# Performance work log

Measured on AMD Instinct MI355X. Metric: run time of the kernel, lower is better.

## Reference

```python
import jax, jax.numpy as jnp
import numpy as np

H = 8  # heads hardcoded in LightGFormer


def layernorm(x, g, b, eps=1e-5):
    m = x.mean(-1, keepdims=True)
    v = ((x - m) ** 2).mean(-1, keepdims=True)
    return (x - m) / jnp.sqrt(v + eps) * g + b


def setup_inputs() -> dict:
    key = jax.random.key(0)
    B, N, D, L = 16, 512, 256, 4
    Dff = 4 * D
    ks = jax.random.split(key, 12)

    def w(k, shape, scale=0.02):
        return jax.random.normal(k, shape, jnp.float32) * scale

    return {
        "input": w(ks[0], (B, N, D), 1.0),
        "input_v": w(ks[1], (B, N, D), 1.0),
        "pos_emb": w(ks[2], (N, D)),
        "Wq": w(ks[3], (L, D, D)), "bq": jnp.zeros((L, D), jnp.float32),
        "Wk": w(ks[4], (L, D, D)), "bk": jnp.zeros((L, D), jnp.float32),
        "Wv": w(ks[5], (L, D, D)), "bv": jnp.zeros((L, D), jnp.float32),
        "Wo": w(ks[6], (L, D, D)), "bo": jnp.zeros((L, D), jnp.float32),
        "W1": w(ks[7], (L, D, Dff)), "b1": jnp.zeros((L, Dff), jnp.float32),
        "W2": w(ks[8], (L, Dff // 2, D // 2)), "b2": jnp.zeros((L, D // 2), jnp.float32),
        "g1": jnp.ones((L, D), jnp.float32), "be1": jnp.zeros((L, D), jnp.float32),
        "g2": jnp.ones((L, D), jnp.float32), "be2": jnp.zeros((L, D), jnp.float32),
        "gf": jnp.ones((D,), jnp.float32), "bf": jnp.zeros((D,), jnp.float32),
        "mask": jax.random.randint(ks[9], (N, N), 0, 2) > 0,
    }


def reference(input, input_v, pos_emb, Wq, bq, Wk, bk, Wv, bv, Wo, bo,
              W1, b1, W2, b2, g1, be1, g2, be2, gf, bf, mask):
    B, N, D = input.shape
    L = Wq.shape[0]
    dk = D // H
    scale = 1.0 / float(np.sqrt(dk))

    x = input + pos_emb[None]       # learned positional encoding
    xv = input_v + pos_emb[None]    # values stream (never updated across layers)

    for i in range(L):
        # --- self-attention: queries/keys from x, values from xv ---
        q = (x @ Wq[i] + bq[i]).reshape(B, N, H, dk)
        k = (x @ Wk[i] + bk[i]).reshape(B, N, H, dk)
        v = (xv @ Wv[i] + bv[i]).reshape(B, N, H, dk)
        att = jnp.einsum('bqhd,bkhd->bhqk', q, k) * scale
        if i % 2 == 1:  # odd layers use the mask (Lightformer alternation)
            att = jnp.where(mask[None, None], -jnp.inf, att)
        att = jax.nn.softmax(att, axis=-1)
        o = jnp.einsum('bhqk,bkhd->bqhd', att, v).reshape(B, N, D)
        o = o @ Wo[i] + bo[i]
        x = layernorm(x + o, g1[i], be1[i])
        # --- FFN with grouped second linear: [.., 2, 2D] @ [2D, D/2] ---
        h = jax.nn.gelu(x @ W1[i] + b1[i], approximate=False)
        h = (h.reshape(B, N, 2, 2 * D) @ W2[i] + b2[i]).reshape(B, N, D)
        x = layernorm(x + h, g2[i], be2[i])

    x = layernorm(x, gf, bf)  # final attention_norm
    return x
```

## Files before the change

### kernel.cpp

```cpp
#include <hip/hip_runtime.h>
#include <hip/hip_bf16.h>
#include <math.h>

#define BDIM 16
#define NSEQ 512
#define DMODEL 256
#define NLAYER 4
#define NHEAD 8
#define DK 32
#define DFF 1024
#define BN (BDIM * NSEQ)
#define ND (NSEQ * DMODEL)

typedef __bf16 bf16x8 __attribute__((ext_vector_type(8)));
typedef float floatx4 __attribute__((ext_vector_type(4)));
typedef unsigned uint32x2 __attribute__((ext_vector_type(2)));

static __device__ __forceinline__ unsigned short f2bf(float f) {
    unsigned u = __float_as_uint(f);
    unsigned r = (u + 0x7FFFu + ((u >> 16) & 1u)) >> 16;
    return (unsigned short)r;
}
static __device__ __forceinline__ float bf2f(unsigned short u) {
    return __uint_as_float(((unsigned)u) << 16);
}

static __device__ __forceinline__ void async_ld16(const unsigned short* g,
                                                  unsigned short* l) {
    __builtin_amdgcn_global_load_lds(
        (const __attribute__((address_space(1))) unsigned int*)g,
        (__attribute__((address_space(3))) unsigned int*)l, 16, 0, 0);
}

static __device__ __forceinline__ float gelu_f(float c) {
    float u = 0.7978845608028654f * (c + 0.044715f * c * c * c);
    return c * (1.f / (1.f + __expf(-2.f * u)));
}

static __device__ __forceinline__ unsigned cvtpk(float lo, float hi) {
    unsigned r;
    asm("v_cvt_pk_bf16_f32 %0, %1, %2" : "=v"(r) : "v"(lo), "v"(hi));
    return r;
}

__global__ void conv_all_kernel(const float* __restrict__ Wq, const float* __restrict__ Wk,
                                const float* __restrict__ Wv, const float* __restrict__ Wo,
                                const float* __restrict__ W1, const float* __restrict__ W2,
                                const int* __restrict__ mask,
                                unsigned short* __restrict__ wqT, unsigned short* __restrict__ wkT,
                                unsigned short* __restrict__ wvT,
                                unsigned short* __restrict__ wo_s,
                                unsigned short* __restrict__ w1_s, unsigned short* __restrict__ w2_s,
                                unsigned* __restrict__ bits) {
    int blk = blockIdx.x, tid = threadIdx.x;
    if (blk < 3072) {
        int i = blk * 256 + tid;
        int sel = i >> 18;
        int j = i & 262143;
        int l = j >> 16, rem = j & 65535, kk = rem >> 8, n = rem & 255;
        const float* src = sel == 0 ? Wq : sel == 1 ? Wk : Wv;
        unsigned short* dst = sel == 0 ? wqT : sel == 1 ? wkT : wvT;
        dst[(size_t)l * 65536 + n * 256 + kk] = f2bf(src[j]);
    } else if (blk < 4096) {
        int i = (blk - 3072) * 256 + tid;
        int l = i >> 16, o = i & 65535;
        int j = o & 7, quad = (o >> 3) & 3, l16 = (o >> 5) & 15;
        int kt = (o >> 9) & 7, cg = (o >> 12) & 15;
        int k = kt * 32 + (j >> 2) * 16 + quad * 4 + (j & 3);
        int dout = cg * 16 + l16;
        wo_s[(size_t)l * 65536 + o] = f2bf(Wo[(size_t)l * 65536 + k * 256 + dout]);
    } else if (blk < 8192) {
        int i = (blk - 4096) * 256 + tid;
        int l = i >> 18, o = i & 262143;
        int j = o & 7, quad = (o >> 3) & 3, l16 = (o >> 5) & 15;
        int kt = (o >> 9) & 7, cg = (o >> 12) & 63;
        int k = kt * 32 + (j >> 2) * 16 + quad * 4 + (j & 3);
        int dout = cg * 16 + l16;
        w1_s[(size_t)l * 262144 + o] = f2bf(W1[(size_t)l * 262144 + k * 1024 + dout]);
    } else if (blk < 9216) {
        int i = (blk - 8192) * 256 + tid;
        int l = i >> 16, o = i & 65535;
        int j = o & 7, quad = (o >> 3) & 3, l16 = (o >> 5) & 15;
        int kt = (o >> 9) & 15, cg = (o >> 13) & 7;
        int k = kt * 32 + (j >> 2) * 16 + quad * 4 + (j & 3);
        int dout = cg * 16 + l16;
        w2_s[(size_t)l * 65536 + o] = f2bf(W2[(size_t)l * 65536 + k * 128 + dout]);
    } else {
        int w = (blk - 9216) * 256 + tid;
        int r = w >> 4, wi = w & 15;
        const int* src = mask + r * NSEQ + wi * 32;
        unsigned acc = 0;
#pragma unroll
        for (int j = 0; j < 32; j++) acc |= (src[j] != 0 ? 1u : 0u) << j;
        bits[w] = acc;
    }
}

__global__ void add_pos_kernel(const float* __restrict__ in,
                               const float* __restrict__ inv,
                               const float* __restrict__ pos,
                               float* __restrict__ x,
                               unsigned short* __restrict__ xb,
                               unsigned short* __restrict__ xvb,
                               int total) {
    int i = blockIdx.x * blockDim.x + threadIdx.x;
    if (i < total) {
        float pe = pos[i % ND];
        float a = in[i] + pe;
        float b = inv[i] + pe;
        x[i] = a;
        xb[i] = f2bf(a);
        xvb[i] = f2bf(b);
    }
}

__global__ __launch_bounds__(256) void qkv_mfma_kernel(
        const unsigned short* __restrict__ xb,
        const unsigned short* __restrict__ xvb,
        const unsigned short* __restrict__ WqT, const unsigned short* __restrict__ WkT,
        const unsigned short* __restrict__ WvT,
        const float* __restrict__ bq, const float* __restrict__ bk,
        const float* __restrict__ bv,
        unsigned short* __restrict__ qo, unsigned short* __restrict__ ko,
        unsigned short* __restrict__ vo) {
    int proj = blockIdx.x >> 1;
    const unsigned short* A  = (proj == 2) ? xvb : xb;
    const unsigned short* Bt = (proj == 0) ? WqT : (proj == 1) ? WkT : WvT;
    const float* bias        = (proj == 0) ? bq  : (proj == 1) ? bk  : bv;
    unsigned short* Cb       = (proj == 0) ? qo  : (proj == 1) ? ko  : vo;
    float qscale = (proj == 0) ? 0.17677669529663687f : 1.f;

    __shared__ unsigned short As[128 * 32];
    __shared__ unsigned short Bs[128 * 32];
    int tid = threadIdx.x;
    int wave = tid >> 6, lane = tid & 63;
    int rowBase = blockIdx.y * 128, colBase = (blockIdx.x & 1) * 128;
    int m0w = (wave & 1) * 64, n0w = (wave >> 1) * 64;
    int lr = lane & 15, quad = lane >> 4;
    int qx = quad ^ (lr & 3);

    floatx4 acc[4][4];
#pragma unroll
    for (int mi = 0; mi < 4; mi++)
#pragma unroll
        for (int nj = 0; nj < 4; nj++) acc[mi][nj] = (floatx4)0.0f;

    for (int kt = 0; kt < DMODEL; kt += 32) {
#pragma unroll
        for (int t = 0; t < 2; t++) {
            int idx = t * 256 + tid;
            int row = idx >> 2, kv8 = ((idx ^ row) & 3) * 8;
            async_ld16(A + (size_t)(rowBase + row) * DMODEL + kt + kv8, &As[idx * 8]);
            async_ld16(Bt + (size_t)(colBase + row) * DMODEL + kt + kv8, &Bs[idx * 8]);
        }
        __syncthreads();
        bf16x8 af[4], bfr[4];
#pragma unroll
        for (int mi = 0; mi < 4; mi++)
            af[mi] = *(const bf16x8*)&As[(m0w + mi * 16 + lr) * 32 + qx * 8];
#pragma unroll
        for (int nj = 0; nj < 4; nj++)
            bfr[nj] = *(const bf16x8*)&Bs[(n0w + nj * 16 + lr) * 32 + qx * 8];
#pragma unroll
        for (int mi = 0; mi < 4; mi++)
#pragma unroll
            for (int nj = 0; nj < 4; nj++)
                acc[mi][nj] = __builtin_amdgcn_mfma_f32_16x16x32_bf16(
                    af[mi], bfr[nj], acc[mi][nj], 0, 0, 0);
        __syncthreads();
    }

#pragma unroll
    for (int mi = 0; mi < 4; mi++) {
#pragma unroll
        for (int r = 0; r < 4; r++) {
            int grow = rowBase + m0w + mi * 16 + quad * 4 + r;
#pragma unroll
            for (int nj = 0; nj < 4; nj++) {
                int gcol = colBase + n0w + nj * 16 + lr;
                float c = (acc[mi][nj][r] + bias[gcol]) * qscale;
                size_t off = ((size_t)((grow >> 9) * 8 + (gcol >> 5)) << 14)
                           + (size_t)(grow & 511) * 32 + (gcol & 31);
                Cb[off] = f2bf(c);
            }
        }
    }
}

__global__ __launch_bounds__(256) void ffn_fused_kernel(
        const unsigned short* __restrict__ ab_f,
        const unsigned short* __restrict__ wo_s,
        const unsigned short* __restrict__ w1_s,
        const unsigned short* __restrict__ w2_s,
        const float* __restrict__ bo,
        const float* __restrict__ g1, const float* __restrict__ be1,
        const float* __restrict__ b1,
        const float* __restrict__ b2,
        const float* __restrict__ g2, const float* __restrict__ be2,
        const float* __restrict__ gf, const float* __restrict__ bf_,
        float* __restrict__ xf, unsigned short* __restrict__ xb,
        float* __restrict__ outF, int finalize) {
    __shared__ unsigned short X1s[8 * 512];
    __shared__ unsigned short Hs[16 * 512];
    __shared__ float redA[16][4], redB[16][4];
    __shared__ float redC[16][4], redD[16][4];
    __shared__ float redE[16][4], redF[16][4];

    int tid = threadIdx.x;
    int w = tid >> 6, lane = tid & 63, l16 = lane & 15, quad = lane >> 4;
    int bid = blockIdx.x;
    int rowBase = bid * 16;
    int fo = (l16 * 4 + quad) * 8;

#define TR2(d0, d1, addr)                                                  \
    asm volatile("ds_read_b64_tr_b16 %0, %2\n\t"                           \
                 "ds_read_b64_tr_b16 %1, %2 offset:512"                    \
                 : "=&v"(d0), "=&v"(d1) : "v"(addr))

    float x0r[4][4];
#pragma unroll
    for (int r = 0; r < 4; r++)
#pragma unroll
        for (int cg = 0; cg < 4; cg++)
            x0r[r][cg] = xf[(size_t)(rowBase + quad * 4 + r) * 256 + w * 64 + cg * 16 + l16];

    floatx4 accA[4];
#pragma unroll
    for (int cg = 0; cg < 4; cg++) accA[cg] = (floatx4)0.0f;

    bf16x8 afA, afAn, bwA[4], bwAn[4];
    afA = *(const bf16x8*)(ab_f + ((size_t)bid * 8 + 0) * 512 + fo);
#pragma unroll
    for (int cg = 0; cg < 4; cg++)
        bwA[cg] = *(const bf16x8*)(wo_s + ((size_t)((w * 4 + cg) * 8 + 0)) * 512 + fo);

#pragma unroll
    for (int kt = 0; kt < 8; kt++) {
        if (kt < 7) {
            afAn = *(const bf16x8*)(ab_f + ((size_t)bid * 8 + kt + 1) * 512 + fo);
#pragma unroll
            for (int cg = 0; cg < 4; cg++)
                bwAn[cg] = *(const bf16x8*)(wo_s + ((size_t)((w * 4 + cg) * 8 + kt + 1)) * 512 + fo);
        }
#pragma unroll
        for (int cg = 0; cg < 4; cg++)
            accA[cg] = __builtin_amdgcn_mfma_f32_16x16x32_bf16(afA, bwA[cg], accA[cg], 0, 0, 0);
        if (kt < 7) {
            afA = afAn;
#pragma unroll
            for (int cg = 0; cg < 4; cg++) bwA[cg] = bwAn[cg];
        }
    }

#pragma unroll
    for (int r = 0; r < 4; r++) {
        int tok = quad * 4 + r;
        float s = 0.f, s2 = 0.f;
#pragma unroll
        for (int cg = 0; cg < 4; cg++) {
            int col = w * 64 + cg * 16 + l16;
            float v = accA[cg][r] + bo[col] + x0r[r][cg];
            accA[cg][r] = v; s += v; s2 += v * v;
        }
#pragma unroll
        for (int off = 1; off <= 8; off <<= 1) {
            s += __shfl_xor(s, off);
            s2 += __shfl_xor(s2, off);
        }
        if (l16 == 0) { redA[tok][w] = s; redB[tok][w] = s2; }
    }
    __syncthreads();
#pragma unroll
    for (int r = 0; r < 4; r++) {
        int tok = quad * 4 + r;
        float ts = redA[tok][0] + redA[tok][1] + redA[tok][2] + redA[tok][3];
        float tq = redB[tok][0] + redB[tok][1] + redB[tok][2] + redB[tok][3];
        float mean = ts * (1.f / 256.f);
        float var = tq * (1.f / 256.f) - mean * mean;
        float rstd = rsqrtf(var + 1e-5f);
#pragma unroll
        for (int cg = 0; cg < 4; cg++) {
            int col = w * 64 + cg * 16 + l16;
            accA[cg][r] = (accA[cg][r] - mean) * rstd * g1[col] + be1[col];
        }
    }
#pragma unroll
    for (int cg = 0; cg < 4; cg++) {
        int col = w * 64 + cg * 16 + l16;
        int ct = col >> 5, colL = col & 31;
        uint32x2 pk;
        pk[0] = cvtpk(accA[cg][0], accA[cg][1]);
        pk[1] = cvtpk(accA[cg][2], accA[cg][3]);
        *(uint32x2*)&X1s[ct * 512 + colL * 16 + quad * 4] = pk;
    }
    __syncthreads();

    unsigned x1addr = (unsigned)(size_t)&X1s[0] + (unsigned)(lane * 8);
    unsigned haddr  = (unsigned)(size_t)&Hs[0]  + (unsigned)(lane * 8);

    floatx4 y[2][2];
#pragma unroll
    for (int g = 0; g < 2; g++)
#pragma unroll
        for (int cj = 0; cj < 2; cj++) y[g][cj] = (floatx4)0.0f;

    for (int g = 0; g < 2; g++) {
        floatx4 accB[8];
#pragma unroll
        for (int c = 0; c < 8; c++) accB[c] = (floatx4)0.0f;

        uint32x2 ta, tb;
        TR2(ta, tb, x1addr);
        bf16x8 bwB[8], bwBn[8];
#pragma unroll
        for (int c = 0; c < 8; c++)
            bwB[c] = *(const bf16x8*)(w1_s +
                ((size_t)((g * 32 + w * 8 + c) * 8 + 0)) * 512 + fo);

#pragma unroll
        for (int kt = 0; kt < 8; kt++) {
            if (kt < 7) {
#pragma unroll
                for (int c = 0; c < 8; c++)
                    bwBn[c] = *(const bf16x8*)(w1_s +
                        ((size_t)((g * 32 + w * 8 + c) * 8 + kt + 1)) * 512 + fo);
            }
            asm volatile("s_waitcnt lgkmcnt(0)");
            __builtin_amdgcn_sched_barrier(0);
            union { bf16x8 v8; uint32x2 u[2]; } afu;
            afu.u[0] = ta; afu.u[1] = tb;
            bf16x8 af = afu.v8;
            if (kt < 7) TR2(ta, tb, x1addr + (unsigned)((kt + 1) * 1024));
#pragma unroll
            for (int c = 0; c < 8; c++)
                accB[c] = __builtin_amdgcn_mfma_f32_16x16x32_bf16(af, bwB[c], accB[c], 0, 0, 0);
            if (kt < 7) {
#pragma unroll
                for (int c = 0; c < 8; c++) bwB[c] = bwBn[c];
            }
        }
#pragma unroll
        for (int c = 0; c < 8; c++) {
            int col = w * 128 + c * 16 + l16;
            float bb = b1[g * 512 + col];
            float o0 = gelu_f(accB[c][0] + bb);
            float o1 = gelu_f(accB[c][1] + bb);
            float o2 = gelu_f(accB[c][2] + bb);
            float o3 = gelu_f(accB[c][3] + bb);
            int ct = col >> 5, colL = col & 31;
            uint32x2 pk;
            pk[0] = cvtpk(o0, o1);
            pk[1] = cvtpk(o2, o3);
            *(uint32x2*)&Hs[ct * 512 + colL * 16 + quad * 4] = pk;
        }
        __syncthreads();

        TR2(ta, tb, haddr);
        bf16x8 bwC[2], bwCn[2];
#pragma unroll
        for (int cj = 0; cj < 2; cj++)
            bwC[cj] = *(const bf16x8*)(w2_s +
                ((size_t)((w * 2 + cj) * 16 + 0)) * 512 + fo);

#pragma unroll
        for (int kt = 0; kt < 16; kt++) {
            if (kt < 15) {
#pragma unroll
                for (int cj = 0; cj < 2; cj++)
                    bwCn[cj] = *(const bf16x8*)(w2_s +
                        ((size_t)((w * 2 + cj) * 16 + kt + 1)) * 512 + fo);
            }
            asm volatile("s_waitcnt lgkmcnt(0)");
            __builtin_amdgcn_sched_barrier(0);
            union { bf16x8 v8; uint32x2 u[2]; } afu;
            afu.u[0] = ta; afu.u[1] = tb;
            bf16x8 af = afu.v8;
            if (kt < 15) TR2(ta, tb, haddr + (unsigned)((kt + 1) * 1024));
#pragma unroll
            for (int cj = 0; cj < 2; cj++)
                y[g][cj] = __builtin_amdgcn_mfma_f32_16x16x32_bf16(af, bwC[cj], y[g][cj], 0, 0, 0);
            if (kt < 15) {
#pragma unroll
                for (int cj = 0; cj < 2; cj++) bwC[cj] = bwCn[cj];
            }
        }
        if (g == 0) __syncthreads();
    }
#undef TR2

#pragma unroll
    for (int r = 0; r < 4; r++) {
        int tok = quad * 4 + r;
        float s = 0.f, s2 = 0.f;
#pragma unroll
        for (int g = 0; g < 2; g++)
#pragma unroll
            for (int cj = 0; cj < 2; cj++) {
                int cc = (w * 2 + cj) * 16 + l16;
                int col = g * 128 + cc;
                float x1v = bf2f(X1s[(col >> 5) * 512 + (col & 31) * 16 + tok]);
                float v = y[g][cj][r] + b2[cc] + x1v;
                y[g][cj][r] = v; s += v; s2 += v * v;
            }
#pragma unroll
        for (int off = 1; off <= 8; off <<= 1) {
            s += __shfl_xor(s, off);
            s2 += __shfl_xor(s2, off);
        }
        if (l16 == 0) { redC[tok][w] = s; redD[tok][w] = s2; }
    }
    __syncthreads();

    if (!finalize) {
#pragma unroll
        for (int r = 0; r < 4; r++) {
            int tok = quad * 4 + r;
            float ts = redC[tok][0] + redC[tok][1] + redC[tok][2] + redC[tok][3];
            float tq = redD[tok][0] + redD[tok][1] + redD[tok][2] + redD[tok][3];
            float mean = ts * (1.f / 256.f);
            float var = tq * (1.f / 256.f) - mean * mean;
            float rstd = rsqrtf(var + 1e-5f);
#pragma unroll
            for (int g = 0; g < 2; g++)
#pragma unroll
                for (int cj = 0; cj < 2; cj++) {
                    int col = g * 128 + (w * 2 + cj) * 16 + l16;
                    float o = (y[g][cj][r] - mean) * rstd * g2[col] + be2[col];
                    xf[(size_t)(rowBase + tok) * 256 + col] = o;
                    xb[(size_t)(rowBase + tok) * 256 + col] = f2bf(o);
                }
        }
    } else {
#pragma unroll
        for (int r = 0; r < 4; r++) {
            int tok = quad * 4 + r;
            float ts = redC[tok][0] + redC[tok][1] + redC[tok][2] + redC[tok][3];
            float tq = redD[tok][0] + redD[tok][1] + redD[tok][2] + redD[tok][3];
            float mean = ts * (1.f / 256.f);
            float var = tq * (1.f / 256.f) - mean * mean;
            float rstd = rsqrtf(var + 1e-5f);
            float s3 = 0.f, q3 = 0.f;
#pragma unroll
            for (int g = 0; g < 2; g++)
#pragma unroll
                for (int cj = 0; cj < 2; cj++) {
                    int col = g * 128 + (w * 2 + cj) * 16 + l16;
                    float o = (y[g][cj][r] - mean) * rstd * g2[col] + be2[col];
                    y[g][cj][r] = o; s3 += o; q3 += o * o;
                }
#pragma unroll
            for (int off = 1; off <= 8; off <<= 1) {
                s3 += __shfl_xor(s3, off);
                q3 += __shfl_xor(q3, off);
            }
            if (l16 == 0) { redE[tok][w] = s3; redF[tok][w] = q3; }
        }
        __syncthreads();
#pragma unroll
        for (int r = 0; r < 4; r++) {
            int tok = quad * 4 + r;
            float ts = redE[tok][0] + redE[tok][1] + redE[tok][2] + redE[tok][3];
            float tq = redF[tok][0] + redF[tok][1] + redF[tok][2] + redF[tok][3];
            float mean = ts * (1.f / 256.f);
            float var = tq * (1.f / 256.f) - mean * mean;
            float rstd = rsqrtf(var + 1e-5f);
#pragma unroll
            for (int g = 0; g < 2; g++)
#pragma unroll
                for (int cj = 0; cj < 2; cj++) {
                    int col = g * 128 + (w * 2 + cj) * 16 + l16;
                    outF[(size_t)(rowBase + tok) * 256 + col]
                        = (y[g][cj][r] - mean) * rstd * gf[col] + bf_[col];
                }
        }
    }
}

__global__ __launch_bounds__(256, 4) void attn_mfma_kernel(
        const unsigned short* __restrict__ q, const unsigned short* __restrict__ k,
        const unsigned short* __restrict__ v, unsigned short* __restrict__ ab_f,
        const unsigned* __restrict__ mbits_g, int use_mask) {
    int bid = blockIdx.x;
    int qg = bid >> 7;
    int bh = bid & 127;
    int h = bh & 7, b = bh >> 3;
    int tid = threadIdx.x;

    __shared__ unsigned short Vs[2][NSEQ * 16];

    const unsigned short* kbase = k + (size_t)(b * 8 + h) * (NSEQ * DK);
    const unsigned short* vbase = v + (size_t)(b * 8 + h) * (NSEQ * DK);

#pragma unroll
    for (int db = 0; db < 2; db++) {
#pragma unroll
        for (int t = 0; t < 4; t++) {
            int c = t * 256 + tid;
            int kk = c >> 1, half = c & 1;
            async_ld16(vbase + (size_t)kk * 32 + db * 16 + half * 8,
                       &Vs[db][c * 8]);
        }
    }

    int wave = tid >> 6, lane = tid & 63, l16 = lane & 15, quad = lane >> 4;
    int qbase = qg * 64 + wave * 16;

    bf16x8 qf = *(const bf16x8*)(q + ((size_t)(b * 8 + h) * NSEQ + qbase + l16) * 32 + quad * 8);

    unsigned mw[16];
    if (use_mask) {
        const uint4* mr = (const uint4*)(mbits_g + (size_t)(qbase + l16) * 16);
#pragma unroll
        for (int w = 0; w < 4; w++) *(uint4*)&mw[w * 4] = mr[w];
    } else {
#pragma unroll
        for (int w = 0; w < 16; w++) mw[w] = 0;
    }
    __syncthreads();

    unsigned va0 = (unsigned)(size_t)&Vs[0][0] + (unsigned)(lane * 8);
    unsigned va1 = (unsigned)(size_t)&Vs[1][0] + (unsigned)(lane * 8);

    const unsigned short* kfrag = kbase + (size_t)l16 * DK + quad * 8;

    floatx4 oT0 = (floatx4)0.f, oT1 = (floatx4)0.f;
    float m_run = -INFINITY, l_part = 0.f;

    uint32x2 t00, t01, t10, t11;
#define TR_ISSUE(cc)                                                      \
    asm volatile("ds_read_b64_tr_b16 %0, %4\n\t"                          \
                 "ds_read_b64_tr_b16 %1, %4 offset:512\n\t"               \
                 "ds_read_b64_tr_b16 %2, %5\n\t"                          \
                 "ds_read_b64_tr_b16 %3, %5 offset:512"                   \
                 : "=&v"(t00), "=&v"(t01), "=&v"(t10), "=&v"(t11)         \
                 : "v"(va0 + (unsigned)((cc) * 1024)),                    \
                   "v"(va1 + (unsigned)((cc) * 1024)))
    TR_ISSUE(0);

    bf16x8 k0 = *(const bf16x8*)(kfrag);
    bf16x8 k1 = *(const bf16x8*)(kfrag + 16 * DK);

#pragma unroll
    for (int c = 0; c < 16; c++) {
        floatx4 s0 = __builtin_amdgcn_mfma_f32_16x16x32_bf16(k0, qf, (floatx4)0.f, 0, 0, 0);
        floatx4 s1 = __builtin_amdgcn_mfma_f32_16x16x32_bf16(k1, qf, (floatx4)0.f, 0, 0, 0);

        bf16x8 k0n, k1n;
        if (c < 15) {
            k0n = *(const bf16x8*)(kfrag + (size_t)((c + 1) * 32) * DK);
            k1n = *(const bf16x8*)(kfrag + (size_t)((c + 1) * 32 + 16) * DK);
        }

        float sv[8];
#pragma unroll
        for (int r = 0; r < 4; r++) { sv[r] = s0[r]; sv[4 + r] = s1[r]; }
        if (use_mask) {
            unsigned wb = mw[c];
#pragma unroll
            for (int r = 0; r < 4; r++) {
                if ((wb >> (quad * 4 + r)) & 1) sv[r] = -INFINITY;
                if ((wb >> (16 + quad * 4 + r)) & 1) sv[4 + r] = -INFINITY;
            }
        }
        float mx = fmaxf(fmaxf(fmaxf(sv[0], sv[1]), fmaxf(sv[2], sv[3])),
                         fmaxf(fmaxf(sv[4], sv[5]), fmaxf(sv[6], sv[7])));
        mx = fmaxf(mx, __shfl_xor(mx, 16));
        mx = fmaxf(mx, __shfl_xor(mx, 32));
        if (!__all(mx <= m_run)) {
            float mnew = fmaxf(m_run, mx);
            float corr = (m_run == mnew) ? 1.f : __expf(m_run - mnew);
            l_part *= corr;
            oT0 *= corr; oT1 *= corr;
            m_run = mnew;
        }
        float p[8];
#pragma unroll
        for (int j = 0; j < 8; j++) {
            float e = __expf(sv[j] - m_run);
            p[j] = (sv[j] > -INFINITY) ? e : 0.f;
            l_part += p[j];
        }
        union { bf16x8 v8; unsigned u[4]; } pf;
#pragma unroll
        for (int j = 0; j < 4; j++)
            pf.u[j] = cvtpk(p[2 * j], p[2 * j + 1]);

        asm volatile("s_waitcnt lgkmcnt(0)");
        __builtin_amdgcn_sched_barrier(0);
        union { bf16x8 v8; uint32x2 u[2]; } av0, av1;
        av0.u[0] = t00; av0.u[1] = t01;
        av1.u[0] = t10; av1.u[1] = t11;

        oT0 = __builtin_amdgcn_mfma_f32_16x16x32_bf16(av0.v8, pf.v8, oT0, 0, 0, 0);
        oT1 = __builtin_amdgcn_mfma_f32_16x16x32_bf16(av1.v8, pf.v8, oT1, 0, 0, 0);
        if (c < 15) TR_ISSUE(c + 1);
        k0 = k0n; k1 = k1n;
    }
#undef TR_ISSUE

    float l = l_part;
    l += __shfl_xor(l, 16);
    l += __shfl_xor(l, 32);
    float invl = (l > 0.f) ? 1.f / l : 0.f;

    uint4 val;
    val.x = cvtpk(oT0[0] * invl, oT0[1] * invl);
    val.y = cvtpk(oT0[2] * invl, oT0[3] * invl);
    val.z = cvtpk(oT1[0] * invl, oT1[1] * invl);
    val.w = cvtpk(oT1[2] * invl, oT1[3] * invl);
    size_t panel = (size_t)b * 32 + qg * 4 + wave;
    *(uint4*)(ab_f + (panel * 8 + h) * 512 + (l16 * 4 + quad) * 8) = val;
}

extern "C" void kernel_launch(void* const* d_in, const int* in_sizes, int n_in,
                              void* d_out, int out_size, void* d_ws, size_t ws_size,
                              hipStream_t stream) {
    const float* input  = (const float*)d_in[0];
    const float* inputv = (const float*)d_in[1];
    const float* pos    = (const float*)d_in[2];
    const float* Wq = (const float*)d_in[3];
    const float* bq = (const float*)d_in[4];
    const float* Wk = (const float*)d_in[5];
    const float* bk = (const float*)d_in[6];
    const float* Wv = (const float*)d_in[7];
    const float* bv = (const float*)d_in[8];
    const float* Wo = (const float*)d_in[9];
    const float* bo = (const float*)d_in[10];
    const float* W1 = (const float*)d_in[11];
    const float* b1 = (const float*)d_in[12];
    const float* W2 = (const float*)d_in[13];
    const float* b2 = (const float*)d_in[14];
    const float* g1 = (const float*)d_in[15];
    const float* be1 = (const float*)d_in[16];
    const float* g2 = (const float*)d_in[17];
    const float* be2 = (const float*)d_in[18];
    const float* gf = (const float*)d_in[19];
    const float* bff = (const float*)d_in[20];
    const int* mask = (const int*)d_in[21];

    float* out = (float*)d_out;

    char* wsb = (char*)d_ws;
    float* x_f  = (float*)(wsb + ((size_t)0 << 20));
    unsigned short* x_b  = (unsigned short*)(wsb + ((size_t)8 << 20));
    unsigned short* xv_b = (unsigned short*)(wsb + ((size_t)12 << 20));
    unsigned short* qb_b = (unsigned short*)(wsb + ((size_t)16 << 20));
    unsigned short* kb_b = (unsigned short*)(wsb + ((size_t)20 << 20));
    unsigned short* vb_b = (unsigned short*)(wsb + ((size_t)24 << 20));
    unsigned short* ab_f = (unsigned short*)(wsb + ((size_t)28 << 20));
    unsigned short* wqT = (unsigned short*)(wsb + ((size_t)32 << 20));
    unsigned short* wkT = wqT + (size_t)4 * 65536;
    unsigned short* wvT = wkT + (size_t)4 * 65536;
    unsigned short* wo_s = wvT + (size_t)4 * 65536;
    unsigned short* w1_s = wo_s + (size_t)4 * 65536;
    unsigned short* w2_s = w1_s + (size_t)4 * 262144;
    unsigned* mbits = (unsigned*)(wsb + ((size_t)37 << 20));

    const size_t TOK = (size_t)BN * DMODEL;

    conv_all_kernel<<<9248, 256, 0, stream>>>(Wq, Wk, Wv, Wo, W1, W2, mask,
                                              wqT, wkT, wvT, wo_s, w1_s, w2_s, mbits);
    add_pos_kernel<<<(int)((TOK + 255) / 256), 256, 0, stream>>>(
        input, inputv, pos, x_f, x_b, xv_b, (int)TOK);

    for (int i = 0; i < NLAYER; i++) {
        const unsigned short* WqT_i = wqT + (size_t)i * 65536;
        const unsigned short* WkT_i = wkT + (size_t)i * 65536;
        const unsigned short* WvT_i = wvT + (size_t)i * 65536;
        const unsigned short* Wo_i  = wo_s + (size_t)i * 65536;
        const unsigned short* W1_i  = w1_s + (size_t)i * 262144;
        const unsigned short* W2_i  = w2_s + (size_t)i * 65536;

        qkv_mfma_kernel<<<dim3(6, 64), 256, 0, stream>>>(
            x_b, xv_b, WqT_i, WkT_i, WvT_i,
            bq + i * DMODEL, bk + i * DMODEL, bv + i * DMODEL,
            qb_b, kb_b, vb_b);

        attn_mfma_kernel<<<BDIM * NHEAD * 8, 256, 0, stream>>>(
            qb_b, kb_b, vb_b, ab_f, mbits, (i & 1));

        ffn_fused_kernel<<<BN / 16, 256, 0, stream>>>(
            ab_f, Wo_i, W1_i, W2_i,
            bo + i * DMODEL, g1 + i * DMODEL, be1 + i * DMODEL,
            b1 + i * DFF, b2 + i * (DMODEL / 2),
            g2 + i * DMODEL, be2 + i * DMODEL,
            gf, bff, x_f, x_b, out, (i == NLAYER - 1) ? 1 : 0);
    }
}
```

Baseline: 405.5 us.

## Split fused FFN kernel work across eight waves per block instead of four

Doubles the fused Wo/LN/FFN kernel block size from 256 to 512 threads, so each of eight waves computes half as many output columns in every GEMM stage. The LayerNorm reductions are widened to eight per-wave partials. Per-column parameters (biases, gammas, betas) are now loaded once into registers up front instead of being re-read inside the epilogues. This is meant to add latency hiding and parallelism for a grid of only 512 blocks. The cost is that each wave's weight loads and shared A-fragment reads are now amortised over fewer MFMAs.

Result: no change. 398.6 us (-1.7%).

```diff
diff --git a/kernel.cpp b/kernel.cpp
--- a/kernel.cpp
+++ b/kernel.cpp
@@ -187,7 +187,7 @@
     }
 }
 
-__global__ __launch_bounds__(256) void ffn_fused_kernel(
+__global__ __launch_bounds__(512) void ffn_fused_kernel(
         const unsigned short* __restrict__ ab_f,
         const unsigned short* __restrict__ wo_s,
         const unsigned short* __restrict__ w1_s,
@@ -202,9 +202,9 @@
         float* __restrict__ outF, int finalize) {
     __shared__ unsigned short X1s[8 * 512];
     __shared__ unsigned short Hs[16 * 512];
-    __shared__ float redA[16][4], redB[16][4];
-    __shared__ float redC[16][4], redD[16][4];
-    __shared__ float redE[16][4], redF[16][4];
+    __shared__ float redA[16][8], redB[16][8];
+    __shared__ float redC[16][8], redD[16][8];
+    __shared__ float redE[16][8], redF[16][8];
 
     int tid = threadIdx.x;
     int w = tid >> 6, lane = tid & 63, l16 = lane & 15, quad = lane >> 4;
@@ -217,38 +217,54 @@
                  "ds_read_b64_tr_b16 %1, %2 offset:512"                    \
                  : "=&v"(d0), "=&v"(d1) : "v"(addr))
 
-    float x0r[4][4];
+    float bo_r[2], g1_r[2], be1_r[2], g2_r[2], be2_r[2], gf_r[2], bfr_[2];
+#pragma unroll
+    for (int cg = 0; cg < 2; cg++) {
+        int colA = w * 32 + cg * 16 + l16;
+        bo_r[cg] = bo[colA]; g1_r[cg] = g1[colA]; be1_r[cg] = be1[colA];
+        int colC = cg * 128 + w * 16 + l16;
+        g2_r[cg] = g2[colC]; be2_r[cg] = be2[colC];
+        gf_r[cg] = gf[colC]; bfr_[cg] = bf_[colC];
+    }
+    float b1_r[2][4];
+#pragma unroll
+    for (int g = 0; g < 2; g++)
+#pragma unroll
+        for (int c = 0; c < 4; c++)
+            b1_r[g][c] = b1[g * 512 + w * 64 + c * 16 + l16];
+    float b2_r = b2[w * 16 + l16];
+    float x0r[4][2];
 #pragma unroll
     for (int r = 0; r < 4; r++)
 #pragma unroll
-        for (int cg = 0; cg < 4; cg++)
-            x0r[r][cg] = xf[(size_t)(rowBase + quad * 4 + r) * 256 + w * 64 + cg * 16 + l16];
-
-    floatx4 accA[4];
-#pragma unroll
-    for (int cg = 0; cg < 4; cg++) accA[cg] = (floatx4)0.0f;
-
-    bf16x8 afA, afAn, bwA[4], bwAn[4];
+        for (int cg = 0; cg < 2; cg++)
+            x0r[r][cg] = xf[(size_t)(rowBase + quad * 4 + r) * 256 + w * 32 + cg * 16 + l16];
+
+    floatx4 accA[2];
+#pragma unroll
+    for (int cg = 0; cg < 2; cg++) accA[cg] = (floatx4)0.0f;
+
+    bf16x8 afA, afAn, bwA[2], bwAn[2];
     afA = *(const bf16x8*)(ab_f + ((size_t)bid * 8 + 0) * 512 + fo);
 #pragma unroll
-    for (int cg = 0; cg < 4; cg++)
-        bwA[cg] = *(const bf16x8*)(wo_s + ((size_t)((w * 4 + cg) * 8 + 0)) * 512 + fo);
+    for (int cg = 0; cg < 2; cg++)
+        bwA[cg] = *(const bf16x8*)(wo_s + ((size_t)((w * 2 + cg) * 8 + 0)) * 512 + fo);
 
 #pragma unroll
     for (int kt = 0; kt < 8; kt++) {
         if (kt < 7) {
             afAn = *(const bf16x8*)(ab_f + ((size_t)bid * 8 + kt + 1) * 512 + fo);
 #pragma unroll
-            for (int cg = 0; cg < 4; cg++)
-                bwAn[cg] = *(const bf16x8*)(wo_s + ((size_t)((w * 4 + cg) * 8 + kt + 1)) * 512 + fo);
-        }
-#pragma unroll
-        for (int cg = 0; cg < 4; cg++)
+            for (int cg = 0; cg < 2; cg++)
+                bwAn[cg] = *(const bf16x8*)(wo_s + ((size_t)((w * 2 + cg) * 8 + kt + 1)) * 512 + fo);
+        }
+#pragma unroll
+        for (int cg = 0; cg < 2; cg++)
             accA[cg] = __builtin_amdgcn_mfma_f32_16x16x32_bf16(afA, bwA[cg], accA[cg], 0, 0, 0);
         if (kt < 7) {
             afA = afAn;
 #pragma unroll
-            for (int cg = 0; cg < 4; cg++) bwA[cg] = bwAn[cg];
+            for (int cg = 0; cg < 2; cg++) bwA[cg] = bwAn[cg];
         }
     }
 
@@ -257,9 +273,8 @@
         int tok = quad * 4 + r;
         float s = 0.f, s2 = 0.f;
 #pragma unroll
-        for (int cg = 0; cg < 4; cg++) {
-            int col = w * 64 + cg * 16 + l16;
-            float v = accA[cg][r] + bo[col] + x0r[r][cg];
+        for (int cg = 0; cg < 2; cg++) {
+            float v = accA[cg][r] + bo_r[cg] + x0r[r][cg];
             accA[cg][r] = v; s += v; s2 += v * v;
         }
 #pragma unroll
@@ -273,57 +288,51 @@
 #pragma unroll
     for (int r = 0; r < 4; r++) {
         int tok = quad * 4 + r;
-        float ts = redA[tok][0] + redA[tok][1] + redA[tok][2] + redA[tok][3];
-        float tq = redB[tok][0] + redB[tok][1] + redB[tok][2] + redB[tok][3];
+        float ts = 0.f, tq = 0.f;
+#pragma unroll
+        for (int ww = 0; ww < 8; ww++) { ts += redA[tok][ww]; tq += redB[tok][ww]; }
         float mean = ts * (1.f / 256.f);
         float var = tq * (1.f / 256.f) - mean * mean;
         float rstd = rsqrtf(var + 1e-5f);
 #pragma unroll
-        for (int cg = 0; cg < 4; cg++) {
-            int col = w * 64 + cg * 16 + l16;
-            accA[cg][r] = (accA[cg][r] - mean) * rstd * g1[col] + be1[col];
-        }
-    }
-#pragma unroll
-    for (int cg = 0; cg < 4; cg++) {
-        int col = w * 64 + cg * 16 + l16;
-        int ct = col >> 5, colL = col & 31;
+        for (int cg = 0; cg < 2; cg++)
+            accA[cg][r] = (accA[cg][r] - mean) * rstd * g1_r[cg] + be1_r[cg];
+    }
+#pragma unroll
+    for (int cg = 0; cg < 2; cg++) {
         uint32x2 pk;
         pk[0] = cvtpk(accA[cg][0], accA[cg][1]);
         pk[1] = cvtpk(accA[cg][2], accA[cg][3]);
-        *(uint32x2*)&X1s[ct * 512 + colL * 16 + quad * 4] = pk;
+        *(uint32x2*)&X1s[w * 512 + (cg * 16 + l16) * 16 + quad * 4] = pk;
     }
     __syncthreads();
 
     unsigned x1addr = (unsigned)(size_t)&X1s[0] + (unsigned)(lane * 8);
     unsigned haddr  = (unsigned)(size_t)&Hs[0]  + (unsigned)(lane * 8);
 
-    floatx4 y[2][2];
-#pragma unroll
-    for (int g = 0; g < 2; g++)
-#pragma unroll
-        for (int cj = 0; cj < 2; cj++) y[g][cj] = (floatx4)0.0f;
+    floatx4 y[2];
+    y[0] = (floatx4)0.0f; y[1] = (floatx4)0.0f;
 
     for (int g = 0; g < 2; g++) {
-        floatx4 accB[8];
-#pragma unroll
-        for (int c = 0; c < 8; c++) accB[c] = (floatx4)0.0f;
+        floatx4 accB[4];
+#pragma unroll
+        for (int c = 0; c < 4; c++) accB[c] = (floatx4)0.0f;
 
         uint32x2 ta, tb;
         TR2(ta, tb, x1addr);
-        bf16x8 bwB[8], bwBn[8];
-#pragma unroll
-        for (int c = 0; c < 8; c++)
+        bf16x8 bwB[4], bwBn[4];
+#pragma unroll
+        for (int c = 0; c < 4; c++)
             bwB[c] = *(const bf16x8*)(w1_s +
-                ((size_t)((g * 32 + w * 8 + c) * 8 + 0)) * 512 + fo);
+                ((size_t)((g * 32 + w * 4 + c) * 8 + 0)) * 512 + fo);
 
 #pragma unroll
         for (int kt = 0; kt < 8; kt++) {
             if (kt < 7) {
 #pragma unroll
-                for (int c = 0; c < 8; c++)
+                for (int c = 0; c < 4; c++)
                     bwBn[c] = *(const bf16x8*)(w1_s +
-                        ((size_t)((g * 32 + w * 8 + c) * 8 + kt + 1)) * 512 + fo);
+                        ((size_t)((g * 32 + w * 4 + c) * 8 + kt + 1)) * 512 + fo);
             }
             asm volatile("s_waitcnt lgkmcnt(0)");
             __builtin_amdgcn_sched_barrier(0);
@@ -332,22 +341,21 @@
             bf16x8 af = afu.v8;
             if (kt < 7) TR2(ta, tb, x1addr + (unsigned)((kt + 1) * 1024));
 #pragma unroll
-            for (int c = 0; c < 8; c++)
+            for (int c = 0; c < 4; c++)
                 accB[c] = __builtin_amdgcn_mfma_f32_16x16x32_bf16(af, bwB[c], accB[c], 0, 0, 0);
             if (kt < 7) {
 #pragma unroll
-                for (int c = 0; c < 8; c++) bwB[c] = bwBn[c];
-            }
-        }
-#pragma unroll
-        for (int c = 0; c < 8; c++) {
-            int col = w * 128 + c * 16 + l16;
-            float bb = b1[g * 512 + col];
+                for (int c = 0; c < 4; c++) bwB[c] = bwBn[c];
+            }
+        }
+#pragma unroll
+        for (int c = 0; c < 4; c++) {
+            float bb = b1_r[g][c];
             float o0 = gelu_f(accB[c][0] + bb);
             float o1 = gelu_f(accB[c][1] + bb);
             float o2 = gelu_f(accB[c][2] + bb);
             float o3 = gelu_f(accB[c][3] + bb);
-            int ct = col >> 5, colL = col & 31;
+            int ct = w * 2 + (c >> 1), colL = (c & 1) * 16 + l16;
             uint32x2 pk;
             pk[0] = cvtpk(o0, o1);
             pk[1] = cvtpk(o2, o3);
@@ -356,33 +364,21 @@
         __syncthreads();
 
         TR2(ta, tb, haddr);
-        bf16x8 bwC[2], bwCn[2];
-#pragma unroll
-        for (int cj = 0; cj < 2; cj++)
-            bwC[cj] = *(const bf16x8*)(w2_s +
-                ((size_t)((w * 2 + cj) * 16 + 0)) * 512 + fo);
+        bf16x8 bwC, bwCn;
+        bwC = *(const bf16x8*)(w2_s + ((size_t)(w * 16 + 0)) * 512 + fo);
 
 #pragma unroll
         for (int kt = 0; kt < 16; kt++) {
-            if (kt < 15) {
-#pragma unroll
-                for (int cj = 0; cj < 2; cj++)
-                    bwCn[cj] = *(const bf16x8*)(w2_s +
-                        ((size_t)((w * 2 + cj) * 16 + kt + 1)) * 512 + fo);
-            }
+            if (kt < 15)
+                bwCn = *(const bf16x8*)(w2_s + ((size_t)(w * 16 + kt + 1)) * 512 + fo);
             asm volatile("s_waitcnt lgkmcnt(0)");
             __builtin_amdgcn_sched_barrier(0);
             union { bf16x8 v8; uint32x2 u[2]; } afu;
             afu.u[0] = ta; afu.u[1] = tb;
             bf16x8 af = afu.v8;
             if (kt < 15) TR2(ta, tb, haddr + (unsigned)((kt + 1) * 1024));
-#pragma unroll
-            for (int cj = 0; cj < 2; cj++)
-                y[g][cj] = __builtin_amdgcn_mfma_f32_16x16x32_bf16(af, bwC[cj], y[g][cj], 0, 0, 0);
-            if (kt < 15) {
-#pragma unroll
-                for (int cj = 0; cj < 2; cj++) bwC[cj] = bwCn[cj];
-            }
+            y[g] = __builtin_amdgcn_mfma_f32_16x16x32_bf16(af, bwC, y[g], 0, 0, 0);
+            if (kt < 15) bwC = bwCn;
         }
         if (g == 0) __syncthreads();
     }
@@ -393,15 +389,12 @@
         int tok = quad * 4 + r;
         float s = 0.f, s2 = 0.f;
 #pragma unroll
-        for (int g = 0; g < 2; g++)
-#pragma unroll
-            for (int cj = 0; cj < 2; cj++) {
-                int cc = (w * 2 + cj) * 16 + l16;
-                int col = g * 128 + cc;
-                float x1v = bf2f(X1s[(col >> 5) * 512 + (col & 31) * 16 + tok]);
-                float v = y[g][cj][r] + b2[cc] + x1v;
-                y[g][cj][r] = v; s += v; s2 += v * v;
-            }
+        for (int g = 0; g < 2; g++) {
+            int col = g * 128 + w * 16 + l16;
+            float x1v = bf2f(X1s[(col >> 5) * 512 + (col & 31) * 16 + tok]);
+            float v = y[g][r] + b2_r + x1v;
+            y[g][r] = v; s += v; s2 += v * v;
+        }
 #pragma unroll
         for (int off = 1; off <= 8; off <<= 1) {
             s += __shfl_xor(s, off);
@@ -415,39 +408,36 @@
 #pragma unroll
         for (int r = 0; r < 4; r++) {
             int tok = quad * 4 + r;
-            float ts = redC[tok][0] + redC[tok][1] + redC[tok][2] + redC[tok][3];
-            float tq = redD[tok][0] + redD[tok][1] + redD[tok][2] + redD[tok][3];
+            float ts = 0.f, tq = 0.f;
+#pragma unroll
+            for (int ww = 0; ww < 8; ww++) { ts += redC[tok][ww]; tq += redD[tok][ww]; }
             float mean = ts * (1.f / 256.f);
             float var = tq * (1.f / 256.f) - mean * mean;
             float rstd = rsqrtf(var + 1e-5f);
 #pragma unroll
-            for (int g = 0; g < 2; g++)
-#pragma unroll
-                for (int cj = 0; cj < 2; cj++) {
-                    int col = g * 128 + (w * 2 + cj) * 16 + l16;
-                    float o = (y[g][cj][r] - mean) * rstd * g2[col] + be2[col];
-                    xf[(size_t)(rowBase + tok) * 256 + col] = o;
-                    xb[(size_t)(rowBase + tok) * 256 + col] = f2bf(o);
-                }
+            for (int g = 0; g < 2; g++) {
+                int col = g * 128 + w * 16 + l16;
+                float o = (y[g][r] - mean) * rstd * g2_r[g] + be2_r[g];
+                xf[(size_t)(rowBase + tok) * 256 + col] = o;
+                xb[(size_t)(rowBase + tok) * 256 + col] = f2bf(o);
+            }
         }
     } else {
 #pragma unroll
         for (int r = 0; r < 4; r++) {
             int tok = quad * 4 + r;
-            float ts = redC[tok][0] + redC[tok][1] + redC[tok][2] + redC[tok][3];
-            float tq = redD[tok][0] + redD[tok][1] + redD[tok][2] + redD[tok][3];
+            float ts = 0.f, tq = 0.f;
+#pragma unroll
+            for (int ww = 0; ww < 8; ww++) { ts += redC[tok][ww]; tq += redD[tok][ww]; }
             float mean = ts * (1.f / 256.f);
             float var = tq * (1.f / 256.f) - mean * mean;
             float rstd = rsqrtf(var + 1e-5f);
             float s3 = 0.f, q3 = 0.f;
 #pragma unroll
-            for (int g = 0; g < 2; g++)
-#pragma unroll
-                for (int cj = 0; cj < 2; cj++) {
-                    int col = g * 128 + (w * 2 + cj) * 16 + l16;
-                    float o = (y[g][cj][r] - mean) * rstd * g2[col] + be2[col];
-                    y[g][cj][r] = o; s3 += o; q3 += o * o;
-                }
+            for (int g = 0; g < 2; g++) {
+                float o = (y[g][r] - mean) * rstd * g2_r[g] + be2_r[g];
+                y[g][r] = o; s3 += o; q3 += o * o;
+            }
 #pragma unroll
             for (int off = 1; off <= 8; off <<= 1) {
                 s3 += __shfl_xor(s3, off);
@@ -459,19 +449,18 @@
 #pragma unroll
         for (int r = 0; r < 4; r++) {
             int tok = quad * 4 + r;
-            float ts = redE[tok][0] + redE[tok][1] + redE[tok][2] + redE[tok][3];
-            float tq = redF[tok][0] + redF[tok][1] + redF[tok][2] + redF[tok][3];
+            float ts = 0.f, tq = 0.f;
+#pragma unroll
+            for (int ww = 0; ww < 8; ww++) { ts += redE[tok][ww]; tq += redF[tok][ww]; }
             float mean = ts * (1.f / 256.f);
             float var = tq * (1.f / 256.f) - mean * mean;
             float rstd = rsqrtf(var + 1e-5f);
 #pragma unroll
-            for (int g = 0; g < 2; g++)
-#pragma unroll
-                for (int cj = 0; cj < 2; cj++) {
-                    int col = g * 128 + (w * 2 + cj) * 16 + l16;
-                    outF[(size_t)(rowBase + tok) * 256 + col]
-                        = (y[g][cj][r] - mean) * rstd * gf[col] + bf_[col];
-                }
+            for (int g = 0; g < 2; g++) {
+                int col = g * 128 + w * 16 + l16;
+                outF[(size_t)(rowBase + tok) * 256 + col]
+                    = (y[g][r] - mean) * rstd * gf_r[g] + bfr_[g];
+            }
         }
     }
 }
@@ -679,7 +668,7 @@
         attn_mfma_kernel<<<BDIM * NHEAD * 8, 256, 0, stream>>>(
             qb_b, kb_b, vb_b, ab_f, mbits, (i & 1));
 
-        ffn_fused_kernel<<<BN / 16, 256, 0, stream>>>(
+        ffn_fused_kernel<<<BN / 16, 512, 0, stream>>>(
             ab_f, Wo_i, W1_i, W2_i,
             bo + i * DMODEL, g1 + i * DMODEL, be1 + i * DMODEL,
             b1 + i * DFF, b2 + i * (DMODEL / 2),
```
